# Performance work log

Measured on AMD Instinct MI355X. Metric: run time of the kernel, lower is better.

## Reference

```python
import jax, jax.numpy as jnp
import numpy as np

N_NODES = 100000
N_EDGES = 1600000
F_IN, HID = 256, 256
HID_OUT = HID // 2  # last SAGE layer output


def _glorot(key, shape):
    fan_in, fan_out = shape[1], shape[0]
    lim = (6.0 / (fan_in + fan_out)) ** 0.5
    return jax.random.uniform(key, shape, jnp.float32, -lim, lim)


def setup_inputs() -> dict:
    key = jax.random.key(0)
    ks = jax.random.split(key, 12)
    x = jax.random.normal(ks[0], (N_NODES, F_IN), jnp.float32)
    edge_index = jax.random.randint(ks[1], (2, N_EDGES), 0, N_NODES, jnp.int64)
    # SAGEConv params: lin_l (on aggregated neighbors, has bias), lin_r (on root)
    dims = [(F_IN, HID), (HID, HID), (HID, HID_OUT)]
    inp = {"x": x, "edge_index": edge_index}
    for i, (din, dout) in enumerate(dims):
        inp[f"Wl{i}"] = _glorot(ks[2 + 3 * i], (dout, din))
        inp[f"Wr{i}"] = _glorot(ks[3 + 3 * i], (dout, din))
        inp[f"b{i}"] = jnp.zeros((dout,), jnp.float32)
    inp["Wc"] = _glorot(ks[11], (1, HID_OUT))
    inp["bc"] = jnp.zeros((1,), jnp.float32)
    return inp


def _sage_conv(x, src, dst, Wl, Wr, b):
    # mean aggregation of source features at destination nodes
    msg_sum = jax.ops.segment_sum(x[src], dst, num_segments=N_NODES)  # [N, d]
    deg = jax.ops.segment_sum(jnp.ones((src.shape[0], 1), x.dtype), dst,
                              num_segments=N_NODES)  # [N, 1]
    agg = msg_sum / jnp.maximum(deg, 1.0)
    return agg @ Wl.T + x @ Wr.T + b


def reference(x, edge_index, Wl0, Wr0, b0, Wl1, Wr1, b1, Wl2, Wr2, b2, Wc, bc):
    src, dst = edge_index[0], edge_index[1]
    layers = [(Wl0, Wr0, b0), (Wl1, Wr1, b1), (Wl2, Wr2, b2)]
    h = x
    for i, (Wl, Wr, b) in enumerate(layers):
        h = _sage_conv(h, src, dst, Wl, Wr, b)
        if i < len(layers) - 1:
            h = jax.nn.relu(h)  # dropout is identity in eval mode
    return jax.nn.sigmoid(h @ Wc.T + bc)  # [N, 1]
```

## Files before the change

### kernel.cpp

```cpp
#include <hip/hip_runtime.h>
#include <math.h>

#define N_NODES 100000
#define N_PAD   100352
#define N_EDGES 1600000
#define DIN 256

#define NB 782
#define NC 256
#define CHUNK 6250
#define MT_N (NB * NC)
#define MT_PAD 200448

typedef unsigned short u16;
typedef unsigned char u8;
typedef unsigned int u32;
typedef __attribute__((ext_vector_type(8))) short bf16x8;
typedef __attribute__((ext_vector_type(8))) unsigned short us8;
typedef __attribute__((ext_vector_type(4))) float f32x4;
typedef __attribute__((ext_vector_type(2))) float f32x2;

__device__ __forceinline__ float b2f(u16 u) {
    union { unsigned int i; float f; } c; c.i = ((unsigned int)u) << 16; return c.f;
}
__device__ __forceinline__ u16 f2b(float f) {
    union { float f; unsigned int i; } c; c.f = f;
    unsigned int x = c.i;
    return (u16)((x + 0x7fffu + ((x >> 16) & 1u)) >> 16);
}
__device__ __forceinline__ u8 f32_to_fp8(float v) {
    return (u8)(__builtin_amdgcn_cvt_pk_fp8_f32(v, 0.0f, 0, false) & 0xff);
}
__device__ __forceinline__ void accum16(float* a, uint4 v) {
    unsigned int w[4] = { v.x, v.y, v.z, v.w };
    #pragma unroll
    for (int q = 0; q < 4; ++q) {
        f32x2 lo = __builtin_amdgcn_cvt_pk_f32_fp8(w[q], false);
        f32x2 hi = __builtin_amdgcn_cvt_pk_f32_fp8(w[q], true);
        a[q * 4 + 0] += lo[0]; a[q * 4 + 1] += lo[1];
        a[q * 4 + 2] += hi[0]; a[q * 4 + 3] += hi[1];
    }
}
__device__ __forceinline__ void accum8(float* a, uint2 v) {
    unsigned int w[2] = { v.x, v.y };
    #pragma unroll
    for (int q = 0; q < 2; ++q) {
        f32x2 lo = __builtin_amdgcn_cvt_pk_f32_fp8(w[q], false);
        f32x2 hi = __builtin_amdgcn_cvt_pk_f32_fp8(w[q], true);
        a[q * 4 + 0] += lo[0]; a[q * 4 + 1] += lo[1];
        a[q * 4 + 2] += hi[0]; a[q * 4 + 3] += hi[1];
    }
}

__device__ __forceinline__ void gload_lds16(const u16* g, u16* lds_base) {
    __builtin_amdgcn_global_load_lds(
        (const __attribute__((address_space(1))) void*)g,
        (__attribute__((address_space(3))) void*)lds_base, 16, 0, 0);
}

__device__ __forceinline__ u32 xcd_chunk(u32 orig, u32 nwg) {
    u32 q = nwg >> 3, r = nwg & 7;
    u32 xcd = orig & 7, idx = orig >> 3;
    u32 base = (xcd < r) ? xcd * (q + 1) : r * (q + 1) + (xcd - r) * q;
    return base + idx;
}

__global__ void cvt_hist_kernel(const float* __restrict__ x, u16* __restrict__ xb,
                                u8* __restrict__ x8,
                                const float* __restrict__ Wl0, const float* __restrict__ Wr0,
                                const float* __restrict__ Wl1, const float* __restrict__ Wr1,
                                const float* __restrict__ Wl2, const float* __restrict__ Wr2,
                                u16* __restrict__ wl0, u16* __restrict__ wr0,
                                u16* __restrict__ wl1, u16* __restrict__ wr1,
                                u16* __restrict__ wl2, u16* __restrict__ wr2,
                                const int* __restrict__ dst, int* __restrict__ MT) {
    __shared__ int bins[NB];
    int b = blockIdx.x;
    if (b < NC) {
        const int c = b, tid = threadIdx.x;
        for (int i = tid; i < NB; i += 256) bins[i] = 0;
        __syncthreads();
        const int e0 = c * CHUNK;
        for (int e = e0 + tid; e < e0 + CHUNK; e += 256)
            atomicAdd(&bins[dst[e] >> 7], 1);
        __syncthreads();
        for (int i = tid; i < NB; i += 256) MT[i * NC + c] = bins[i];
        return;
    }
    b -= NC;
    if (b < 320) {
        const float* s; u16* d; int i;
        if (b < 64)       { s = Wl0; d = wl0; i = b * 256 + threadIdx.x; }
        else if (b < 128) { s = Wr0; d = wr0; i = (b - 64) * 256 + threadIdx.x; }
        else if (b < 192) { s = Wl1; d = wl1; i = (b - 128) * 256 + threadIdx.x; }
        else if (b < 256) { s = Wr1; d = wr1; i = (b - 192) * 256 + threadIdx.x; }
        else if (b < 288) { s = Wl2; d = wl2; i = (b - 256) * 256 + threadIdx.x; }
        else              { s = Wr2; d = wr2; i = (b - 288) * 256 + threadIdx.x; }
        float4 v = ((const float4*)s)[i];
        ushort4 o;
        o.x = f2b(v.x); o.y = f2b(v.y); o.z = f2b(v.z); o.w = f2b(v.w);
        ((ushort4*)d)[i] = o;
        return;
    }
    b -= 320;
    int i = b * 256 + threadIdx.x;
    if (i < N_NODES * 64) {
        float4 v = ((const float4*)x)[i];
        ushort4 o;
        o.x = f2b(v.x); o.y = f2b(v.y); o.z = f2b(v.z); o.w = f2b(v.w);
        ((ushort4*)xb)[i] = o;
        u32 r = __builtin_amdgcn_cvt_pk_fp8_f32(v.x, v.y, 0, false);
        r = __builtin_amdgcn_cvt_pk_fp8_f32(v.z, v.w, r, true);
        ((u32*)x8)[i] = r;
    }
}

__global__ void scan1_kernel(const int* __restrict__ in, int* __restrict__ excl,
                             int* __restrict__ blocksums, int n) {
    __shared__ int s[256];
    int tid = threadIdx.x;
    int i = blockIdx.x * 256 + tid;
    int v = (i < n) ? in[i] : 0;
    s[tid] = v;
    __syncthreads();
    for (int off = 1; off < 256; off <<= 1) {
        int t = (tid >= off) ? s[tid - off] : 0;
        __syncthreads();
        s[tid] += t;
        __syncthreads();
    }
    if (i < n) excl[i] = s[tid] - v;
    if (tid == 255) blocksums[blockIdx.x] = s[255];
}

__global__ void scan_carry_kernel(int* __restrict__ bsums, int nb) {
    __shared__ int s[256];
    int tid = threadIdx.x;
    int carry = 0;
    for (int base = 0; base < nb; base += 256) {
        int i = base + tid;
        int v = (i < nb) ? bsums[i] : 0;
        s[tid] = v;
        __syncthreads();
        for (int off = 1; off < 256; off <<= 1) {
            int t = (tid >= off) ? s[tid - off] : 0;
            __syncthreads();
            s[tid] += t;
            __syncthreads();
        }
        int incl = s[tid];
        int tot = s[255];
        if (i < nb) bsums[i] = incl - v + carry;
        carry += tot;
        __syncthreads();
    }
}

__launch_bounds__(256)
__global__ void p2_partition(const int* __restrict__ src, const int* __restrict__ dst,
                             const int* __restrict__ MTs, const int* __restrict__ bsums,
                             u32* __restrict__ csr_tmp) {
    __shared__ int cur[NB];
    const int c = blockIdx.x, tid = threadIdx.x;
    for (int b = tid; b < NB; b += 256) cur[b] = MTs[b * NC + c] + bsums[b];
    __syncthreads();
    const int e0 = c * CHUNK;
    for (int e = e0 + tid; e < e0 + CHUNK; e += 256) {
        int d = dst[e];
        int pos = atomicAdd(&cur[d >> 7], 1);
        csr_tmp[pos] = ((u32)(d & 127) << 25) | (u32)src[e];
    }
}

__launch_bounds__(256)
__global__ void p3_csr(const int* __restrict__ MTs, const int* __restrict__ bsums,
                       const u32* __restrict__ csr_tmp,
                       int* __restrict__ csr, int* __restrict__ rowptr,
                       int* __restrict__ rowend, float* __restrict__ rinv) {
    __shared__ int cnt[128];
    __shared__ int excl[128];
    __shared__ int cur[128];
    const int b = blockIdx.x, tid = threadIdx.x;
    const int beg = MTs[b * NC] + bsums[b];
    const int end = (b == NB - 1) ? N_EDGES : (MTs[(b + 1) * NC] + bsums[b + 1]);
    if (tid < 128) cnt[tid] = 0;
    __syncthreads();
    for (int e = beg + tid; e < end; e += 256)
        atomicAdd(&cnt[csr_tmp[e] >> 25], 1);
    __syncthreads();
    if (tid == 0) {
        int run = 0;
        for (int i = 0; i < 128; ++i) { excl[i] = run; run += cnt[i]; }
    }
    __syncthreads();
    if (tid < 128) cur[tid] = beg + excl[tid];
    __syncthreads();
    for (int e = beg + tid; e < end; e += 256) {
        u32 v = csr_tmp[e];
        int pos = atomicAdd(&cur[v >> 25], 1);
        csr[pos] = (int)(v & 0x1FFFFFFu);
    }
    if (tid < 128) {
        int node = b * 128 + tid;
        if (node < N_NODES) {
            int rp = beg + excl[tid];
            rowptr[node] = rp;
            rowend[node] = rp + cnt[tid];
            rinv[node]   = 1.0f / (float)max(cnt[tid], 1);
        }
    }
}

__launch_bounds__(256)
__global__ void agg_kernel(const int* __restrict__ rowptr, const int* __restrict__ rowend,
                           const int* __restrict__ csr_src, const float* __restrict__ rinv,
                           const u8* __restrict__ h8, u16* __restrict__ agg) {
    int node = blockIdx.x * 16 + (threadIdx.x >> 4);
    int lane = threadIdx.x & 15;
    if (node >= N_NODES) return;
    int beg = rowptr[node];
    int end = rowend[node];
    const u8* hl = h8 + lane * 16;
    float a[16] = {};
    int p = beg;
    for (; p + 3 < end; p += 4) {
        int s0 = csr_src[p], s1 = csr_src[p + 1], s2 = csr_src[p + 2], s3 = csr_src[p + 3];
        uint4 v0 = *(const uint4*)(hl + (size_t)s0 * 256);
        uint4 v1 = *(const uint4*)(hl + (size_t)s1 * 256);
        uint4 v2 = *(const uint4*)(hl + (size_t)s2 * 256);
        uint4 v3 = *(const uint4*)(hl + (size_t)s3 * 256);
        accum16(a, v0); accum16(a, v1); accum16(a, v2); accum16(a, v3);
    }
    for (; p < end; ++p) {
        uint4 v0 = *(const uint4*)(hl + (size_t)csr_src[p] * 256);
        accum16(a, v0);
    }
    float r = rinv[node];
    us8 o0, o1;
    #pragma unroll
    for (int j = 0; j < 8; ++j) { o0[j] = f2b(a[j] * r); o1[j] = f2b(a[8 + j] * r); }
    u16* d = agg + (size_t)node * DIN + lane * 16;
    *(us8*)d = o0;
    *(us8*)(d + 8) = o1;
}

template <int MODE>
__launch_bounds__(256)
__global__ void sage_gemm(const u16* __restrict__ A0, const u16* __restrict__ A1,
                          const u16* __restrict__ B0w, const u16* __restrict__ B1w,
                          const float* __restrict__ bias, void* __restrict__ out0,
                          void* __restrict__ out1, u8* __restrict__ out8,
                          int dout, int do_relu) {
    __shared__ u16 sA[3][128 * 32];
    __shared__ u16 sB[3][128 * 32];

    const u32 u    = xcd_chunk(blockIdx.x, gridDim.x);
    const int csel = u & 1;
    const int row0 = (int)(u >> 1) * 128;
    const int col0 = (MODE == 0) ? csel * 128 : 0;
    const int t    = threadIdx.x;
    const int w    = t >> 6, lane = t & 63;
    const int wr   = w >> 1, wc = w & 1;
    const int lr   = lane & 15, lg = lane >> 4;
    const int srow = lane >> 2;
    const int sblk = (lane & 3) ^ ((lane >> 3) & 3);
    const u16* Bsel = csel ? B1w : B0w;

    f32x4 acc[4][4] = {};
    const int NT = (MODE == 0) ? 16 : 8;

    auto stage = [&](int buf, int tk) {
        const int kt = tk * 32;
        const u16* Asrc = (MODE == 0 && kt >= 256) ? A1 : A0;
        const u16* Bsrc = (MODE == 0) ? ((kt >= 256) ? B1w : B0w) : Bsel;
        const int  kb   = (MODE == 0 && kt >= 256) ? kt - 256 : kt;
        #pragma unroll
        for (int i = 0; i < 2; ++i) {
            int row = w * 32 + i * 16 + srow;
            gload_lds16(Asrc + (size_t)(row0 + row) * DIN + kb + sblk * 8,
                        &sA[buf][w * 1024 + i * 512]);
            gload_lds16(Bsrc + (size_t)(col0 + row) * DIN + kb + sblk * 8,
                        &sB[buf][w * 1024 + i * 512]);
        }
    };

    stage(0, 0);
    stage(1, 1);
    int cur = 0;
    for (int tk = 0; tk < NT; ++tk) {
        if (tk + 1 < NT) asm volatile("s_waitcnt vmcnt(4)" ::: "memory");
        else             asm volatile("s_waitcnt vmcnt(0)" ::: "memory");
        __builtin_amdgcn_sched_barrier(0);
        __builtin_amdgcn_s_barrier();
        __builtin_amdgcn_sched_barrier(0);
        if (tk + 2 < NT) {
            int nb3 = cur - 1; if (nb3 < 0) nb3 = 2;
            stage(nb3, tk + 2);
        }

        bf16x8 af[4], bfr[4];
        #pragma unroll
        for (int m = 0; m < 4; ++m) {
            int row = wr * 64 + m * 16 + lr;
            af[m] = *(const bf16x8*)&sA[cur][row * 32 + 8 * (lg ^ ((lr >> 1) & 3))];
        }
        #pragma unroll
        for (int n = 0; n < 4; ++n) {
            int row = wc * 64 + n * 16 + lr;
            bfr[n] = *(const bf16x8*)&sB[cur][row * 32 + 8 * (lg ^ ((lr >> 1) & 3))];
        }
        #pragma unroll
        for (int m = 0; m < 4; ++m)
            #pragma unroll
            for (int n = 0; n < 4; ++n)
                acc[m][n] = __builtin_amdgcn_mfma_f32_16x16x32_bf16(af[m], bfr[n], acc[m][n], 0, 0, 0);

        cur = (cur == 2) ? 0 : cur + 1;
    }

    const bool f32out = (MODE == 1) && (csel == 1);
    #pragma unroll
    for (int m = 0; m < 4; ++m) {
        int row = row0 + wr * 64 + m * 16 + lg * 4;
        #pragma unroll
        for (int n = 0; n < 4; ++n) {
            int col = col0 + wc * 64 + n * 16 + lr;
            #pragma unroll
            for (int r = 0; r < 4; ++r) {
                float v = acc[m][n][r];
                if (MODE == 0) {
                    v += bias[col];
                    if (do_relu) v = fmaxf(v, 0.0f);
                    ((u16*)out0)[(size_t)(row + r) * dout + col] = f2b(v);
                    if (out8) out8[(size_t)(row + r) * dout + col] = f32_to_fp8(v);
                } else if (f32out) {
                    v += bias[col];
                    ((float*)out1)[(size_t)(row + r) * dout + col] = v;
                } else {
                    out8[(size_t)(row + r) * dout + col] = f32_to_fp8(v);
                }
            }
        }
    }
}

__launch_bounds__(256)
__global__ void aggcls_kernel(const int* __restrict__ rowptr, const int* __restrict__ rowend,
                              const int* __restrict__ csr_src, const float* __restrict__ rinv,
                              const u8* __restrict__ z28, const float* __restrict__ y2,
                              const float* __restrict__ Wc, const float* __restrict__ bc,
                              float* __restrict__ out) {
    __shared__ float sW[128];
    int t = threadIdx.x;
    if (t < 128) sW[t] = Wc[t];
    __syncthreads();
    int node = blockIdx.x * 16 + (t >> 4);
    int lane = t & 15;
    if (node >= N_NODES) return;
    int beg = rowptr[node];
    int end = rowend[node];
    const u8* zl = z28 + lane * 8;
    float a[8] = {};
    int p = beg;
    for (; p + 3 < end; p += 4) {
        int s0 = csr_src[p], s1 = csr_src[p + 1], s2 = csr_src[p + 2], s3 = csr_src[p + 3];
        uint2 v0 = *(const uint2*)(zl + (size_t)s0 * 128);
        uint2 v1 = *(const uint2*)(zl + (size_t)s1 * 128);
        uint2 v2 = *(const uint2*)(zl + (size_t)s2 * 128);
        uint2 v3 = *(const uint2*)(zl + (size_t)s3 * 128);
        accum8(a, v0); accum8(a, v1); accum8(a, v2); accum8(a, v3);
    }
    for (; p < end; ++p) {
        uint2 v0 = *(const uint2*)(zl + (size_t)csr_src[p] * 128);
        accum8(a, v0);
    }
    float r = rinv[node];
    float4 ylo = *(const float4*)(y2 + (size_t)node * 128 + lane * 8);
    float4 yhi = *(const float4*)(y2 + (size_t)node * 128 + lane * 8 + 4);
    float yv[8] = { ylo.x, ylo.y, ylo.z, ylo.w, yhi.x, yhi.y, yhi.z, yhi.w };
    float s = 0.f;
    #pragma unroll
    for (int j = 0; j < 8; ++j)
        s += (a[j] * r + yv[j]) * sW[lane * 8 + j];
    #pragma unroll
    for (int off = 8; off; off >>= 1) s += __shfl_xor(s, off, 16);
    if (lane == 0) {
        float z = s + bc[0];
        out[node] = 1.0f / (1.0f + expf(-z));
    }
}

extern "C" void kernel_launch(void* const* d_in, const int* in_sizes, int n_in,
                              void* d_out, int out_size, void* d_ws, size_t ws_size,
                              hipStream_t stream) {
    const float* x   = (const float*)d_in[0];
    const int*   ei  = (const int*)d_in[1];
    const float* Wl0 = (const float*)d_in[2];
    const float* Wr0 = (const float*)d_in[3];
    const float* b0  = (const float*)d_in[4];
    const float* Wl1 = (const float*)d_in[5];
    const float* Wr1 = (const float*)d_in[6];
    const float* b1  = (const float*)d_in[7];
    const float* Wl2 = (const float*)d_in[8];
    const float* Wr2 = (const float*)d_in[9];
    const float* b2  = (const float*)d_in[10];
    const float* Wc  = (const float*)d_in[11];
    const float* bc  = (const float*)d_in[12];
    float* out = (float*)d_out;

    const int* src = ei;
    const int* dst = ei + N_EDGES;

    int*   MT     = (int*)d_ws;
    int*   MTs    = MT + MT_PAD;
    int*   bsums  = MTs + MT_PAD;
    u32*   csrtmp = (u32*)(bsums + 1024);
    int*   csr    = (int*)(csrtmp + N_EDGES);
    int*   rowptr = csr + N_EDGES;
    int*   rowend = rowptr + N_PAD;
    float* rinv   = (float*)(rowend + N_PAD);
    u16*   xb     = (u16*)(rinv + N_PAD);
    u16*   wb     = xb + (size_t)N_PAD * 256;
    u16*   bufA   = wb + 327680;
    u16*   bufB   = bufA + (size_t)N_PAD * 256;
    u16*   bufC   = bufB + (size_t)N_PAD * 256;
    u8*    x8     = (u8*)(bufC + (size_t)N_PAD * 256);
    u8*    h18    = x8 + (size_t)N_PAD * 256;
    u8*    z28    = h18 + (size_t)N_PAD * 256;

    u16* wl0 = wb;
    u16* wr0 = wl0 + 65536;
    u16* wl1 = wr0 + 65536;
    u16* wr1 = wl1 + 65536;
    u16* wl2 = wr1 + 65536;
    u16* wr2 = wl2 + 32768;

    const int xblocks = (N_NODES * 64 + 255) / 256;
    cvt_hist_kernel<<<NC + 320 + xblocks, 256, 0, stream>>>(
        x, xb, x8, Wl0, Wr0, Wl1, Wr1, Wl2, Wr2,
        wl0, wr0, wl1, wr1, wl2, wr2, dst, MT);

    const int scan_blocks = MT_N / 256;
    scan1_kernel<<<scan_blocks, 256, 0, stream>>>(MT, MTs, bsums, MT_N);
    scan_carry_kernel<<<1, 256, 0, stream>>>(bsums, scan_blocks);
    p2_partition<<<NC, 256, 0, stream>>>(src, dst, MTs, bsums, csrtmp);
    p3_csr<<<NB, 256, 0, stream>>>(MTs, bsums, csrtmp, csr, rowptr, rowend, rinv);

    const int Mblocks = (N_NODES + 127) / 128;
    const int gemm_blocks = Mblocks * 2;
    const int agg_blocks = (N_NODES + 15) / 16;

    agg_kernel<<<agg_blocks, 256, 0, stream>>>(rowptr, rowend, csr, rinv, x8, bufA);
    sage_gemm<0><<<gemm_blocks, 256, 0, stream>>>(bufA, xb, wl0, wr0, b0, bufB, nullptr, h18, 256, 1);

    agg_kernel<<<agg_blocks, 256, 0, stream>>>(rowptr, rowend, csr, rinv, h18, bufA);
    sage_gemm<0><<<gemm_blocks, 256, 0, stream>>>(bufA, bufB, wl1, wr1, b1, bufC, nullptr, nullptr, 256, 1);

    sage_gemm<1><<<gemm_blocks, 256, 0, stream>>>(bufC, nullptr, wl2, wr2, b2, nullptr, bufB, z28, 128, 0);
    aggcls_kernel<<<agg_blocks, 256, 0, stream>>>(rowptr, rowend, csr, rinv,
                                                  z28, (const float*)bufB, Wc, bc, out);
}
```

Baseline: 419.2 us.

## Load GEMM B operand directly to registers and deepen A LDS pipeline

The sage_gemm kernel no longer stages the weight (B) tiles through shared memory. Each wave now loads its B fragments straight from global memory into registers, double-buffered one k-step ahead, while the A tile pipeline in LDS goes from three to four slots. This is meant to halve LDS traffic and LDS footprint, which could allow higher occupancy. The cost is more global loads of weights that were shared across waves (relying on cache hits) and more registers for the B buffers, and the hand-written vmcnt counts must match the new number of loads in flight.

Result: slower. 470.2 us (+12.2%).

```diff
diff --git a/kernel.cpp b/kernel.cpp
--- a/kernel.cpp
+++ b/kernel.cpp
@@ -251,8 +251,7 @@
                           const float* __restrict__ bias, void* __restrict__ out0,
                           void* __restrict__ out1, u8* __restrict__ out8,
                           int dout, int do_relu) {
-    __shared__ u16 sA[3][128 * 32];
-    __shared__ u16 sB[3][128 * 32];
+    __shared__ u16 sA[4][128 * 32];
 
     const u32 u    = xcd_chunk(blockIdx.x, gridDim.x);
     const int csel = u & 1;
@@ -265,57 +264,77 @@
     const int srow = lane >> 2;
     const int sblk = (lane & 3) ^ ((lane >> 3) & 3);
     const u16* Bsel = csel ? B1w : B0w;
+    const int NT = (MODE == 0) ? 16 : 8;
 
     f32x4 acc[4][4] = {};
-    const int NT = (MODE == 0) ? 16 : 8;
-
-    auto stage = [&](int buf, int tk) {
+
+    auto stageA = [&](int slot, int tk) {
         const int kt = tk * 32;
         const u16* Asrc = (MODE == 0 && kt >= 256) ? A1 : A0;
-        const u16* Bsrc = (MODE == 0) ? ((kt >= 256) ? B1w : B0w) : Bsel;
         const int  kb   = (MODE == 0 && kt >= 256) ? kt - 256 : kt;
         #pragma unroll
         for (int i = 0; i < 2; ++i) {
             int row = w * 32 + i * 16 + srow;
             gload_lds16(Asrc + (size_t)(row0 + row) * DIN + kb + sblk * 8,
-                        &sA[buf][w * 1024 + i * 512]);
-            gload_lds16(Bsrc + (size_t)(col0 + row) * DIN + kb + sblk * 8,
-                        &sB[buf][w * 1024 + i * 512]);
+                        &sA[slot][w * 1024 + i * 512]);
         }
     };
-
-    stage(0, 0);
-    stage(1, 1);
-    int cur = 0;
-    for (int tk = 0; tk < NT; ++tk) {
-        if (tk + 1 < NT) asm volatile("s_waitcnt vmcnt(4)" ::: "memory");
-        else             asm volatile("s_waitcnt vmcnt(0)" ::: "memory");
-        __builtin_amdgcn_sched_barrier(0);
-        __builtin_amdgcn_s_barrier();
-        __builtin_amdgcn_sched_barrier(0);
-        if (tk + 2 < NT) {
-            int nb3 = cur - 1; if (nb3 < 0) nb3 = 2;
-            stage(nb3, tk + 2);
-        }
-
-        bf16x8 af[4], bfr[4];
+    auto loadB = [&](int tk, bf16x8* dst) {
+        const int kt = tk * 32;
+        const u16* Bsrc = (MODE == 0) ? ((kt >= 256) ? B1w : B0w) : Bsel;
+        const int kb = (MODE == 0 && kt >= 256) ? kt - 256 : kt;
+        #pragma unroll
+        for (int n = 0; n < 4; ++n)
+            dst[n] = *(const bf16x8*)(Bsrc +
+                (size_t)(col0 + wc * 64 + n * 16 + lr) * DIN + kb + lg * 8);
+    };
+    auto dsreadA = [&](int slot, bf16x8* af) {
         #pragma unroll
         for (int m = 0; m < 4; ++m) {
             int row = wr * 64 + m * 16 + lr;
-            af[m] = *(const bf16x8*)&sA[cur][row * 32 + 8 * (lg ^ ((lr >> 1) & 3))];
-        }
-        #pragma unroll
-        for (int n = 0; n < 4; ++n) {
-            int row = wc * 64 + n * 16 + lr;
-            bfr[n] = *(const bf16x8*)&sB[cur][row * 32 + 8 * (lg ^ ((lr >> 1) & 3))];
-        }
+            af[m] = *(const bf16x8*)&sA[slot][row * 32 + 8 * (lg ^ ((lr >> 1) & 3))];
+        }
+    };
+    auto mfma16 = [&](bf16x8* af, bf16x8* bfr) {
         #pragma unroll
         for (int m = 0; m < 4; ++m)
             #pragma unroll
             for (int n = 0; n < 4; ++n)
                 acc[m][n] = __builtin_amdgcn_mfma_f32_16x16x32_bf16(af[m], bfr[n], acc[m][n], 0, 0, 0);
-
-        cur = (cur == 2) ? 0 : cur + 1;
+    };
+
+    stageA(0, 0); stageA(1, 1); stageA(2, 2);
+    bf16x8 bX[4], bY[4], af[4];
+    loadB(0, bX);
+
+    int cur = 0;
+    for (int tk = 0; tk < NT; tk += 2) {
+        if (tk + 2 < NT)      asm volatile("s_waitcnt vmcnt(8)" ::: "memory");
+        else if (tk + 1 < NT) asm volatile("s_waitcnt vmcnt(6)" ::: "memory");
+        else                  asm volatile("s_waitcnt vmcnt(4)" ::: "memory");
+        __builtin_amdgcn_sched_barrier(0);
+        __builtin_amdgcn_s_barrier();
+        __builtin_amdgcn_sched_barrier(0);
+        if (tk + 1 < NT) loadB(tk + 1, bY);
+        if (tk + 3 < NT) stageA((cur + 3) & 3, tk + 3);
+        dsreadA(cur, af);
+        mfma16(af, bX);
+        cur = (cur + 1) & 3;
+
+        if (tk + 1 < NT) {
+            const int s = tk + 1;
+            if (s + 2 < NT)      asm volatile("s_waitcnt vmcnt(8)" ::: "memory");
+            else if (s + 1 < NT) asm volatile("s_waitcnt vmcnt(6)" ::: "memory");
+            else                 asm volatile("s_waitcnt vmcnt(4)" ::: "memory");
+            __builtin_amdgcn_sched_barrier(0);
+            __builtin_amdgcn_s_barrier();
+            __builtin_amdgcn_sched_barrier(0);
+            if (s + 1 < NT) loadB(s + 1, bX);
+            if (s + 3 < NT) stageA((cur + 3) & 3, s + 3);
+            dsreadA(cur, af);
+            mfma16(af, bY);
+            cur = (cur + 1) & 3;
+        }
     }
 
     const bool f32out = (MODE == 1) && (csel == 1);
```
